# Performance work log

Hardware: AMD Instinct MI355X
Metric: run time of the kernel (lower is better)

Reference implementation:

```python
import jax, jax.numpy as jnp
import numpy as np

K_TOKENS = 40  # safety_token_count
LN_EPS = 1e-5


def setup_inputs() -> dict:
    key = jax.random.key(0)
    ks = jax.random.split(key, 3)
    B, S, D = 16, 4096, 768
    H = D // 2
    features = jax.random.normal(ks[0], (B, S, D), dtype=jnp.float32)
    W1 = jax.random.normal(ks[1], (D, H), dtype=jnp.float32) * (1.0 / np.sqrt(D))
    b1 = jnp.zeros((H,), dtype=jnp.float32)
    ln_gamma = jnp.ones((H,), dtype=jnp.float32)
    ln_beta = jnp.zeros((H,), dtype=jnp.float32)
    W2 = jax.random.normal(ks[2], (H, 1), dtype=jnp.float32) * (1.0 / np.sqrt(H))
    b2 = jnp.zeros((1,), dtype=jnp.float32)
    return {"features": features, "W1": W1, "b1": b1,
            "ln_gamma": ln_gamma, "ln_beta": ln_beta, "W2": W2, "b2": b2}


def _scores(features, W1, b1, ln_gamma, ln_beta, W2, b2):
    # Linear -> LayerNorm -> GELU(exact) -> Dropout(eval=identity) -> Linear -> Sigmoid
    h = jnp.einsum('bsd,dh->bsh', features, W1) + b1
    mu = jnp.mean(h, axis=-1, keepdims=True)
    var = jnp.mean(jnp.square(h - mu), axis=-1, keepdims=True)
    h = (h - mu) * jax.lax.rsqrt(var + LN_EPS) * ln_gamma + ln_beta
    h = jax.nn.gelu(h, approximate=False)
    s = jnp.einsum('bsh,ho->bso', h, W2) + b2  # [B, S, 1]
    return jax.nn.sigmoid(s[..., 0])           # [B, S]


def reference(features, W1, b1, ln_gamma, ln_beta, W2, b2):
    scores = _scores(features, W1, b1, ln_gamma, ln_beta, W2, b2)
    k = min(K_TOKENS, features.shape[1])
    _, indices = jax.lax.top_k(scores, k)                      # [B, k]
    safety_tokens = jnp.take_along_axis(features, indices[:, :, None], axis=1)  # [B, k, D]
    return safety_tokens, indices
```

## Files before the change

### kernel.cpp

```cpp
#include <hip/hip_runtime.h>
#include <math.h>

#define B_   16
#define S_   4096
#define D_   768
#define H_   384
#define NTOK (B_ * S_)
#define KTOP 40
#define NTILES 24
#define KCH    24

typedef __attribute__((ext_vector_type(8))) short bf16x8;
typedef __attribute__((ext_vector_type(4))) float f32x4;

static __device__ __forceinline__ unsigned short f2bf(float x) {
    union { float f; unsigned u; } v; v.f = x;
    unsigned r = v.u + 0x7FFF + ((v.u >> 16) & 1);
    return (unsigned short)(r >> 16);
}
static __device__ __forceinline__ float bf2f(unsigned short h) {
    union { unsigned u; float f; } v; v.u = ((unsigned)h) << 16; return v.f;
}

__global__ __launch_bounds__(64) void pack_w1(const float* __restrict__ W1,
                                              unsigned short* __restrict__ bh,
                                              unsigned short* __restrict__ bl)
{
    const int nt   = blockIdx.x;
    const int ch   = blockIdx.y;
    const int lane = threadIdx.x;
    const int n    = nt * 16 + (lane & 15);
    const int k0   = ch * 32 + (lane >> 4) * 8;

    unsigned short h8[8], l8[8];
#pragma unroll
    for (int j = 0; j < 8; ++j) {
        const float v = W1[(size_t)(k0 + j) * H_ + n];
        const unsigned short h = f2bf(v);
        h8[j] = h;
        l8[j] = f2bf(v - bf2f(h));
    }
    const size_t base = ((size_t)(nt * KCH + ch) * 64 + lane) * 8;
#pragma unroll
    for (int j = 0; j < 8; ++j) { bh[base + j] = h8[j]; bl[base + j] = l8[j]; }
}

__global__ __launch_bounds__(256, 3) void score_kernel(
    const float* __restrict__ features,
    const unsigned short* __restrict__ bh_g,
    const unsigned short* __restrict__ bl_g,
    const float* __restrict__ b1,
    const float* __restrict__ gamma,
    const float* __restrict__ beta,
    const float* __restrict__ W2,
    const float* __restrict__ b2,
    float* __restrict__ scores)
{
    __shared__ unsigned short Ah[32][40];
    __shared__ unsigned short Al[32][40];
    __shared__ float red[4][32];
    __shared__ float mu_s[32];
    __shared__ float rs_s[32];

    const int tid  = threadIdx.x;
    const int lane = tid & 63;
    const int w    = tid >> 6;
    const int base = blockIdx.x * 32;
    const int cl   = lane & 15;
    const int p    = lane >> 4;

    f32x4 acc[2][6];
#pragma unroll
    for (int m = 0; m < 2; ++m)
#pragma unroll
        for (int t = 0; t < 6; ++t) acc[m][t] = (f32x4){0.f, 0.f, 0.f, 0.f};

    const int r0 = tid >> 3, c0 = (tid & 7) * 4;

    float4 p0 = *(const float4*)(features + (size_t)(base + r0) * D_ + c0);

    for (int c = 0; c < KCH; ++c) {
        if (c) __syncthreads();
        {
            unsigned short h0 = f2bf(p0.x), h1 = f2bf(p0.y), h2 = f2bf(p0.z), h3 = f2bf(p0.w);
            Ah[r0][c0] = h0; Ah[r0][c0+1] = h1; Ah[r0][c0+2] = h2; Ah[r0][c0+3] = h3;
            Al[r0][c0]   = f2bf(p0.x - bf2f(h0));
            Al[r0][c0+1] = f2bf(p0.y - bf2f(h1));
            Al[r0][c0+2] = f2bf(p0.z - bf2f(h2));
            Al[r0][c0+3] = f2bf(p0.w - bf2f(h3));
        }
        if (c + 1 < KCH) {
            const int d0 = (c + 1) * 32;
            p0 = *(const float4*)(features + (size_t)(base + r0) * D_ + d0 + c0);
        }
        __syncthreads();

        bf16x8 ahf[2], alf[2];
#pragma unroll
        for (int m = 0; m < 2; ++m) {
            const int row = m * 16 + cl;
            const int k0  = p * 8;
            ahf[m] = *(const bf16x8*)&Ah[row][k0];
            alf[m] = *(const bf16x8*)&Al[row][k0];
        }
#pragma unroll
        for (int t = 0; t < 6; ++t) {
            const size_t bb = ((size_t)((w * 6 + t) * KCH + c) * 64 + lane) * 8;
            const bf16x8 bhf = *(const bf16x8*)(bh_g + bb);
            const bf16x8 blf = *(const bf16x8*)(bl_g + bb);
#pragma unroll
            for (int m = 0; m < 2; ++m) {
                acc[m][t] = __builtin_amdgcn_mfma_f32_16x16x32_bf16(ahf[m], bhf, acc[m][t], 0, 0, 0);
                acc[m][t] = __builtin_amdgcn_mfma_f32_16x16x32_bf16(ahf[m], blf, acc[m][t], 0, 0, 0);
                acc[m][t] = __builtin_amdgcn_mfma_f32_16x16x32_bf16(alf[m], bhf, acc[m][t], 0, 0, 0);
            }
        }
    }

    float b1v[6], gv[6], bev[6], w2v[6];
#pragma unroll
    for (int t = 0; t < 6; ++t) {
        const int n = (w * 6 + t) * 16 + cl;
        b1v[t] = b1[n]; gv[t] = gamma[n]; bev[t] = beta[n]; w2v[t] = W2[n];
    }
#pragma unroll
    for (int m = 0; m < 2; ++m)
#pragma unroll
        for (int t = 0; t < 6; ++t)
#pragma unroll
            for (int r = 0; r < 4; ++r) acc[m][t][r] += b1v[t];

#pragma unroll
    for (int m = 0; m < 2; ++m) {
        float sm[4] = {0.f, 0.f, 0.f, 0.f};
#pragma unroll
        for (int t = 0; t < 6; ++t)
#pragma unroll
            for (int r = 0; r < 4; ++r) sm[r] += acc[m][t][r];
#pragma unroll
        for (int r = 0; r < 4; ++r) {
#pragma unroll
            for (int off = 1; off <= 8; off <<= 1) sm[r] += __shfl_xor(sm[r], off, 64);
        }
        if (cl == 0) {
#pragma unroll
            for (int r = 0; r < 4; ++r) red[w][m * 16 + p * 4 + r] = sm[r];
        }
    }
    __syncthreads();
    if (tid < 32) mu_s[tid] = (red[0][tid] + red[1][tid] + red[2][tid] + red[3][tid]) * (1.0f / H_);
    __syncthreads();

#pragma unroll
    for (int m = 0; m < 2; ++m) {
        float mur[4];
#pragma unroll
        for (int r = 0; r < 4; ++r) mur[r] = mu_s[m * 16 + p * 4 + r];
        float sm[4] = {0.f, 0.f, 0.f, 0.f};
#pragma unroll
        for (int t = 0; t < 6; ++t)
#pragma unroll
            for (int r = 0; r < 4; ++r) { const float d = acc[m][t][r] - mur[r]; sm[r] += d * d; }
#pragma unroll
        for (int r = 0; r < 4; ++r) {
#pragma unroll
            for (int off = 1; off <= 8; off <<= 1) sm[r] += __shfl_xor(sm[r], off, 64);
        }
        if (cl == 0) {
#pragma unroll
            for (int r = 0; r < 4; ++r) red[w][m * 16 + p * 4 + r] = sm[r];
        }
    }
    __syncthreads();
    if (tid < 32) rs_s[tid] = rsqrtf((red[0][tid] + red[1][tid] + red[2][tid] + red[3][tid]) * (1.0f / H_) + 1e-5f);
    __syncthreads();

#pragma unroll
    for (int m = 0; m < 2; ++m) {
        float mur[4], rsr[4];
#pragma unroll
        for (int r = 0; r < 4; ++r) { mur[r] = mu_s[m * 16 + p * 4 + r]; rsr[r] = rs_s[m * 16 + p * 4 + r]; }
        float sm[4] = {0.f, 0.f, 0.f, 0.f};
#pragma unroll
        for (int t = 0; t < 6; ++t)
#pragma unroll
            for (int r = 0; r < 4; ++r) {
                const float y  = (acc[m][t][r] - mur[r]) * rsr[r] * gv[t] + bev[t];
                const float ge = 0.5f * y * (1.0f + erff(y * 0.70710678118654752f));
                sm[r] = fmaf(ge, w2v[t], sm[r]);
            }
#pragma unroll
        for (int r = 0; r < 4; ++r) {
#pragma unroll
            for (int off = 1; off <= 8; off <<= 1) sm[r] += __shfl_xor(sm[r], off, 64);
        }
        if (cl == 0) {
#pragma unroll
            for (int r = 0; r < 4; ++r) red[w][m * 16 + p * 4 + r] = sm[r];
        }
    }
    __syncthreads();
    if (tid < 32) {
        const float s = red[0][tid] + red[1][tid] + red[2][tid] + red[3][tid] + b2[0];
        scores[base + tid] = 1.0f / (1.0f + expf(-s));
    }
}

__global__ __launch_bounds__(256) void select_kernel(const float* __restrict__ scores,
                                                     int* __restrict__ sel)
{
    __shared__ unsigned int bits_s[S_];
    __shared__ unsigned int hist[256];
    __shared__ int s_byte, s_above, s_rem;
    __shared__ unsigned int s_ngt, s_neq;
    __shared__ unsigned int candV[64];
    __shared__ int candI[64];
    __shared__ int eqI[256];

    const int b   = blockIdx.x;
    const int tid = threadIdx.x;

    for (int i = tid; i < S_; i += 256)
        bits_s[i] = __float_as_uint(scores[b * S_ + i]);
    if (tid == 0) { s_rem = KTOP; s_ngt = 0u; s_neq = 0u; }

    unsigned int prefix = 0u, mask = 0u;
    for (int pb = 3; pb >= 0; --pb) {
        hist[tid] = 0u;
        __syncthreads();
        for (int i = tid; i < S_; i += 256) {
            const unsigned int u = bits_s[i];
            if ((u & mask) == prefix) atomicAdd(&hist[(u >> (8 * pb)) & 255u], 1u);
        }
        __syncthreads();
        if (tid == 0) {
            int c = 0, v = 255;
            for (; v >= 0; --v) { c += (int)hist[v]; if (c >= s_rem) break; }
            s_byte  = v;
            s_above = c - (int)hist[v];
            s_rem   = s_rem - s_above;
        }
        __syncthreads();
        prefix |= ((unsigned int)s_byte) << (8 * pb);
        mask   |= 0xFFu << (8 * pb);
        __syncthreads();
    }
    const unsigned int T = prefix;
    const int need = s_rem;

    for (int i = tid; i < S_; i += 256) {
        const unsigned int u = bits_s[i];
        if (u > T) {
            const unsigned int pos = atomicAdd(&s_ngt, 1u);
            candV[pos] = u; candI[pos] = i;
        } else if (u == T) {
            const unsigned int pos = atomicAdd(&s_neq, 1u);
            if (pos < 256u) eqI[pos] = i;
        }
    }
    __syncthreads();
    const int ngt = (int)s_ngt;
    const int neq = (int)(s_neq < 256u ? s_neq : 256u);
    for (int j = tid; j < neq; j += 256) {
        int rank = 0;
        for (int l = 0; l < neq; ++l) rank += (eqI[l] < eqI[j]) ? 1 : 0;
        if (rank < need) { candV[ngt + rank] = T; candI[ngt + rank] = eqI[j]; }
    }
    __syncthreads();
    if (tid < KTOP) {
        const unsigned int u = candV[tid];
        const int idx = candI[tid];
        int rank = 0;
        for (int j = 0; j < KTOP; ++j)
            rank += (candV[j] > u || (candV[j] == u && candI[j] < idx)) ? 1 : 0;
        sel[b * KTOP + rank] = idx;
    }
}

__global__ __launch_bounds__(192) void gather_kernel(const float* __restrict__ features,
                                                     const int* __restrict__ sel,
                                                     float* __restrict__ out_tok,
                                                     float* __restrict__ out_idx)
{
    const int i = blockIdx.x;
    const int b = blockIdx.y;
    const int idx = sel[b * KTOP + i];
    const float4* src = (const float4*)(features + ((size_t)b * S_ + idx) * D_);
    float4* dst = (float4*)(out_tok + ((size_t)b * KTOP + i) * D_);
    dst[threadIdx.x] = src[threadIdx.x];
    if (threadIdx.x == 0) out_idx[b * KTOP + i] = (float)idx;
}

extern "C" void kernel_launch(void* const* d_in, const int* in_sizes, int n_in,
                              void* d_out, int out_size, void* d_ws, size_t ws_size,
                              hipStream_t stream)
{
    const float* features = (const float*)d_in[0];
    const float* W1       = (const float*)d_in[1];
    const float* b1       = (const float*)d_in[2];
    const float* gamma    = (const float*)d_in[3];
    const float* beta     = (const float*)d_in[4];
    const float* W2       = (const float*)d_in[5];
    const float* b2       = (const float*)d_in[6];

    unsigned short* bh = (unsigned short*)d_ws;
    unsigned short* bl = bh + (size_t)D_ * H_;
    float* scores      = (float*)(bl + (size_t)D_ * H_);
    int*   sel         = (int*)(scores + NTOK);

    float* out        = (float*)d_out;
    float* out_tokens = out;
    float* out_idx    = out + (size_t)B_ * KTOP * D_;

    pack_w1<<<dim3(NTILES, KCH), 64, 0, stream>>>(W1, bh, bl);
    score_kernel<<<NTOK / 32, 256, 0, stream>>>(features, bh, bl, b1, gamma, beta, W2, b2, scores);
    select_kernel<<<B_, 256, 0, stream>>>(scores, sel);
    gather_kernel<<<dim3(KTOP, B_), 192, 0, stream>>>(features, sel, out_tokens, out_idx);
}
```

Measured before the change: 457.0 us.

## Multi-buffer A tiles in LDS, raise occupancy, parallelize radix-select scan

```diff
diff --git a/kernel.cpp b/kernel.cpp
--- a/kernel.cpp
+++ b/kernel.cpp
@@ -45,7 +45,7 @@
     for (int j = 0; j < 8; ++j) { bh[base + j] = h8[j]; bl[base + j] = l8[j]; }
 }
 
-__global__ __launch_bounds__(256, 3) void score_kernel(
+__global__ __launch_bounds__(256, 4) void score_kernel(
     const float* __restrict__ features,
     const unsigned short* __restrict__ bh_g,
     const unsigned short* __restrict__ bl_g,
@@ -56,8 +56,8 @@
     const float* __restrict__ b2,
     float* __restrict__ scores)
 {
-    __shared__ unsigned short Ah[32][40];
-    __shared__ unsigned short Al[32][40];
+    __shared__ unsigned short Ah[4][32][40];
+    __shared__ unsigned short Al[4][32][40];
     __shared__ float red[4][32];
     __shared__ float mu_s[32];
     __shared__ float rs_s[32];
@@ -76,46 +76,63 @@
         for (int t = 0; t < 6; ++t) acc[m][t] = (f32x4){0.f, 0.f, 0.f, 0.f};
 
     const int r0 = tid >> 3, c0 = (tid & 7) * 4;
-
-    float4 p0 = *(const float4*)(features + (size_t)(base + r0) * D_ + c0);
-
-    for (int c = 0; c < KCH; ++c) {
-        if (c) __syncthreads();
-        {
-            unsigned short h0 = f2bf(p0.x), h1 = f2bf(p0.y), h2 = f2bf(p0.z), h3 = f2bf(p0.w);
-            Ah[r0][c0] = h0; Ah[r0][c0+1] = h1; Ah[r0][c0+2] = h2; Ah[r0][c0+3] = h3;
-            Al[r0][c0]   = f2bf(p0.x - bf2f(h0));
-            Al[r0][c0+1] = f2bf(p0.y - bf2f(h1));
-            Al[r0][c0+2] = f2bf(p0.z - bf2f(h2));
-            Al[r0][c0+3] = f2bf(p0.w - bf2f(h3));
-        }
-        if (c + 1 < KCH) {
-            const int d0 = (c + 1) * 32;
-            p0 = *(const float4*)(features + (size_t)(base + r0) * D_ + d0 + c0);
-        }
-        __syncthreads();
-
-        bf16x8 ahf[2], alf[2];
-#pragma unroll
-        for (int m = 0; m < 2; ++m) {
-            const int row = m * 16 + cl;
-            const int k0  = p * 8;
-            ahf[m] = *(const bf16x8*)&Ah[row][k0];
-            alf[m] = *(const bf16x8*)&Al[row][k0];
-        }
-#pragma unroll
-        for (int t = 0; t < 6; ++t) {
-            const size_t bb = ((size_t)((w * 6 + t) * KCH + c) * 64 + lane) * 8;
-            const bf16x8 bhf = *(const bf16x8*)(bh_g + bb);
-            const bf16x8 blf = *(const bf16x8*)(bl_g + bb);
+    const float* arow = features + (size_t)(base + r0) * D_ + c0;
+
+#define STAGE(vec, slot)                                                      \
+    do {                                                                      \
+        const float4 _v = (vec);                                              \
+        unsigned short h0 = f2bf(_v.x), h1 = f2bf(_v.y),                      \
+                       h2 = f2bf(_v.z), h3 = f2bf(_v.w);                      \
+        Ah[slot][r0][c0]   = h0; Ah[slot][r0][c0+1] = h1;                     \
+        Ah[slot][r0][c0+2] = h2; Ah[slot][r0][c0+3] = h3;                     \
+        Al[slot][r0][c0]   = f2bf(_v.x - bf2f(h0));                           \
+        Al[slot][r0][c0+1] = f2bf(_v.y - bf2f(h1));                           \
+        Al[slot][r0][c0+2] = f2bf(_v.z - bf2f(h2));                           \
+        Al[slot][r0][c0+3] = f2bf(_v.w - bf2f(h3));                           \
+    } while (0)
+
+    float4 q0 = *(const float4*)(arow + 0 * 32);
+    float4 q1 = *(const float4*)(arow + 1 * 32);
+    STAGE(q0, 0);
+    STAGE(q1, 1);
+    __syncthreads();
+
+    for (int i = 0; i < 12; ++i) {
+        if (i < 11) {
+            q0 = *(const float4*)(arow + (2 * i + 2) * 32);
+            q1 = *(const float4*)(arow + (2 * i + 3) * 32);
+        }
+#pragma unroll
+        for (int s = 0; s < 2; ++s) {
+            const int c    = 2 * i + s;
+            const int slot = c & 3;
+            bf16x8 ahf[2], alf[2];
 #pragma unroll
             for (int m = 0; m < 2; ++m) {
-                acc[m][t] = __builtin_amdgcn_mfma_f32_16x16x32_bf16(ahf[m], bhf, acc[m][t], 0, 0, 0);
-                acc[m][t] = __builtin_amdgcn_mfma_f32_16x16x32_bf16(ahf[m], blf, acc[m][t], 0, 0, 0);
-                acc[m][t] = __builtin_amdgcn_mfma_f32_16x16x32_bf16(alf[m], bhf, acc[m][t], 0, 0, 0);
-            }
-        }
-    }
+                const int row = m * 16 + cl;
+                ahf[m] = *(const bf16x8*)&Ah[slot][row][p * 8];
+                alf[m] = *(const bf16x8*)&Al[slot][row][p * 8];
+            }
+#pragma unroll
+            for (int t = 0; t < 6; ++t) {
+                const size_t bb = ((size_t)((w * 6 + t) * KCH + c) * 64 + lane) * 8;
+                const bf16x8 bhf = *(const bf16x8*)(bh_g + bb);
+                const bf16x8 blf = *(const bf16x8*)(bl_g + bb);
+#pragma unroll
+                for (int m = 0; m < 2; ++m) {
+                    acc[m][t] = __builtin_amdgcn_mfma_f32_16x16x32_bf16(ahf[m], bhf, acc[m][t], 0, 0, 0);
+                    acc[m][t] = __builtin_amdgcn_mfma_f32_16x16x32_bf16(ahf[m], blf, acc[m][t], 0, 0, 0);
+                    acc[m][t] = __builtin_amdgcn_mfma_f32_16x16x32_bf16(alf[m], bhf, acc[m][t], 0, 0, 0);
+                }
+            }
+        }
+        if (i < 11) {
+            STAGE(q0, (2 * i + 2) & 3);
+            STAGE(q1, (2 * i + 3) & 3);
+        }
+        __syncthreads();
+    }
+#undef STAGE
 
     float b1v[6], gv[6], bev[6], w2v[6];
 #pragma unroll
@@ -211,14 +228,18 @@
 {
     __shared__ unsigned int bits_s[S_];
     __shared__ unsigned int hist[256];
-    __shared__ int s_byte, s_above, s_rem;
+    __shared__ unsigned int suf[256];
+    __shared__ unsigned int wtot[4];
+    __shared__ int s_byte, s_rem;
     __shared__ unsigned int s_ngt, s_neq;
     __shared__ unsigned int candV[64];
     __shared__ int candI[64];
     __shared__ int eqI[256];
 
-    const int b   = blockIdx.x;
-    const int tid = threadIdx.x;
+    const int b    = blockIdx.x;
+    const int tid  = threadIdx.x;
+    const int lane = tid & 63;
+    const int w4   = tid >> 6;
 
     for (int i = tid; i < S_; i += 256)
         bits_s[i] = __float_as_uint(scores[b * S_ + i]);
@@ -233,12 +254,27 @@
             if ((u & mask) == prefix) atomicAdd(&hist[(u >> (8 * pb)) & 255u], 1u);
         }
         __syncthreads();
-        if (tid == 0) {
-            int c = 0, v = 255;
-            for (; v >= 0; --v) { c += (int)hist[v]; if (c >= s_rem) break; }
-            s_byte  = v;
-            s_above = c - (int)hist[v];
-            s_rem   = s_rem - s_above;
+        {
+            unsigned int v = hist[tid];
+#pragma unroll
+            for (int off = 1; off < 64; off <<= 1) {
+                const unsigned int y = __shfl_down(v, off, 64);
+                if (lane + off < 64) v += y;
+            }
+            if (lane == 0) wtot[w4] = v;
+            __syncthreads();
+            unsigned int add = 0u;
+#pragma unroll
+            for (int j = 0; j < 4; ++j) if (j > w4) add += wtot[j];
+            v += add;
+            suf[tid] = v;
+            __syncthreads();
+            const int rem = s_rem;
+            const unsigned int nxt = (tid < 255) ? suf[tid + 1] : 0u;
+            if (suf[tid] >= (unsigned)rem && (tid == 255 || nxt < (unsigned)rem)) {
+                s_byte = tid;
+                s_rem  = rem - (int)nxt;
+            }
         }
         __syncthreads();
         prefix |= ((unsigned int)s_byte) << (8 * pb);
```

New measurement: 429.6 us. -6.0%, faster.
